# Kernel optimization log

Measured on AMD Instinct MI355X. Metric: run time of the kernel, lower is better.

## Reference

```python
import jax, jax.numpy as jnp
import numpy as np

N = 200_000   # nodes
E = 6_400_000 # edges (avg degree 32)
F = 128       # input features
H = 8         # latent_dim
G = 1024      # graphs in batch


def setup_inputs() -> dict:
    key = jax.random.key(0)
    ks = jax.random.split(key, 8)
    x = jax.random.normal(ks[0], (N, F), dtype=jnp.float32)
    edge_index = jax.random.randint(ks[1], (2, E), 0, N, dtype=jnp.int64)
    batch = jnp.sort(jax.random.randint(ks[2], (N,), 0, G, dtype=jnp.int64))
    W1 = jax.random.normal(ks[3], (F, H), dtype=jnp.float32) * 0.1
    b1 = jnp.zeros((H,), dtype=jnp.float32)
    W2 = jax.random.normal(ks[4], (H, H), dtype=jnp.float32) * 0.1
    b2 = jnp.zeros((H,), dtype=jnp.float32)
    Wl = jax.random.normal(ks[5], (H, 1), dtype=jnp.float32) * 0.1
    bl = jnp.zeros((1,), dtype=jnp.float32)
    return {"x": x, "W1": W1, "b1": b1, "W2": W2, "b2": b2,
            "Wl": Wl, "bl": bl, "edge_index": edge_index,
            "batch": batch, "num_graphs": G}


def gcn_conv(x, W, b, src, dst, n):
    """PyG GCNConv: add self-loops, symmetric deg^{-1/2} normalization,
    scatter-add aggregation, then bias."""
    loop = jnp.arange(n, dtype=src.dtype)
    s = jnp.concatenate([src, loop])
    d = jnp.concatenate([dst, loop])
    deg = jax.ops.segment_sum(jnp.ones_like(d, dtype=x.dtype), d, num_segments=n)
    dinv = jax.lax.rsqrt(deg)  # deg >= 1 thanks to self-loops
    norm = dinv[s] * dinv[d]   # [E+N]
    h = x @ W                  # [N, H] small GEMM
    msg = h[s] * norm[:, None] # irregular gather over edges
    return jax.ops.segment_sum(msg, d, num_segments=n) + b


def reference(x, W1, b1, W2, b2, Wl, bl, edge_index, batch, num_graphs):
    src, dst = edge_index[0], edge_index[1]
    n = x.shape[0]
    h = jax.nn.relu(gcn_conv(x, W1, b1, src, dst, n))
    h = jax.nn.relu(gcn_conv(h, W2, b2, src, dst, n))
    # per-graph node-sum readout (fused segment_sum replaces the torch loop)
    outs = jax.ops.segment_sum(h, batch, num_segments=num_graphs)  # [G, H]
    logits = outs @ Wl + bl  # [G, 1]
    return jax.nn.sigmoid(logits)
```

## Files before the change

kernel.cpp:

```cpp
#include <hip/hip_runtime.h>
#include <hip/hip_bf16.h>
#include <math.h>

#define THREADS 256
#define SHIFT 8
#define B1 512
#define S1T 1024
#define TILE 8192
#define EPT (TILE / S1T)
#define ECAP 10240
#define BCAP ECAP
#define CPT (ECAP / 512)

typedef _Float16 f16x8 __attribute__((ext_vector_type(8)));
typedef float f32x4 __attribute__((ext_vector_type(4)));

#define NTL(p) __builtin_nontemporal_load(p)

static inline size_t A256(size_t x) { return (x + 255) & ~(size_t)255; }

__global__ void init_kernel(int* __restrict__ gcursor, int NBUK) {
    int i = blockIdx.x * blockDim.x + threadIdx.x;
    if (i < NBUK) gcursor[i] = i * ECAP;
}

__global__ __launch_bounds__(S1T) void scatterd_kernel(
        const int* __restrict__ src, const int* __restrict__ dst,
        int* __restrict__ gcursor, int* __restrict__ ebuf, int E, int chunk) {
    __shared__ int cnt[1024];
    __shared__ int texcl[1024];
    __shared__ int runbase[1024];
    __shared__ int wtot[16];
    __shared__ int spk[TILE];
    __shared__ unsigned short sbk[TILE];
    int b = blockIdx.x, t = threadIdx.x;
    int lane = t & 63, wv = t >> 6;
    int lo = b * chunk, hi = min(E, lo + chunk);
    for (int tb = lo; tb < hi; tb += TILE) {
        int tn = min(TILE, hi - tb);
        cnt[t] = 0;
        __syncthreads();
        int pk[EPT], bk[EPT], rk[EPT];
#pragma unroll
        for (int i = 0; i < EPT; ++i) {
            int idx = t + i * S1T;
            if (idx < tn) {
                int e = tb + idx;
                int s = src[e], d = dst[e];
                bk[i] = d >> SHIFT;
                pk[i] = ((d & 255) << 24) | s;
                rk[i] = atomicAdd(&cnt[bk[i]], 1);
            } else bk[i] = -1;
        }
        __syncthreads();
        int v = cnt[t];
        if (v > 0) runbase[t] = atomicAdd(&gcursor[t], v);
        int inc = v;
#pragma unroll
        for (int m = 1; m < 64; m <<= 1) {
            int u = __shfl_up(inc, m, 64);
            if (lane >= m) inc += u;
        }
        if (lane == 63) wtot[wv] = inc;
        __syncthreads();
        int pre = 0;
        for (int j = 0; j < wv; ++j) pre += wtot[j];
        texcl[t] = pre + inc - v;
        __syncthreads();
#pragma unroll
        for (int i = 0; i < EPT; ++i) {
            if (bk[i] >= 0) {
                int p = texcl[bk[i]] + rk[i];
                spk[p] = pk[i];
                sbk[p] = (unsigned short)bk[i];
            }
        }
        __syncthreads();
        for (int j = t; j < tn; j += S1T) {
            int bkt = sbk[j];
            ebuf[runbase[bkt] + (j - texcl[bkt])] = spk[j];
        }
        __syncthreads();
    }
}

__global__ __launch_bounds__(512) void bucket_csr_kernel(
        const int* __restrict__ ebuf, const int* __restrict__ gcursor,
        int* __restrict__ ebuf2, int2* __restrict__ rowinfo,
        float* __restrict__ dinv, int N) {
    __shared__ int cnt[256];
    __shared__ int cur[256];
    __shared__ int wtot[4];
    __shared__ int srt[BCAP];
    int k = blockIdx.x, t = threadIdx.x;
    int lane = t & 63;
    int bs = k * ECAP;
    int n = min(gcursor[k] - bs, BCAP);
    if (t < 256) cnt[t] = 0;
    __syncthreads();
    int p[CPT], rk[CPT];
#pragma unroll
    for (int u = 0; u < CPT; ++u) {
        int i = t + u * 512;
        if (i < n) {
            p[u] = ebuf[bs + i];
            rk[u] = atomicAdd(&cnt[(p[u] >> 24) & 255], 1);
        }
    }
    __syncthreads();
    int myc = 0, inc = 0;
    if (t < 256) {
        myc = cnt[t];
        inc = myc;
#pragma unroll
        for (int m = 1; m < 64; m <<= 1) {
            int u = __shfl_up(inc, m, 64);
            if (lane >= m) inc += u;
        }
        if (lane == 63) wtot[t >> 6] = inc;
    }
    __syncthreads();
    if (t < 256) {
        int pre = 0;
        for (int j = 0; j < (t >> 6); ++j) pre += wtot[j];
        int ex = pre + inc - myc;
        cur[t] = ex;
        int node = (k << SHIFT) + t;
        if (node < N) {
            rowinfo[node] = make_int2(bs + ex, myc);
            dinv[node] = rsqrtf((float)myc + 1.0f);
        }
    }
    __syncthreads();
#pragma unroll
    for (int u = 0; u < CPT; ++u) {
        int i = t + u * 512;
        if (i < n)
            srt[cur[(p[u] >> 24) & 255] + rk[u]] = p[u] & 0xFFFFFF;
    }
    __syncthreads();
    for (int i = t; i < n; i += 512) ebuf2[bs + i] = srt[i];
}

__global__ __launch_bounds__(256) void gemm1_kernel(
        const float* __restrict__ x, const float* __restrict__ W1,
        const float* __restrict__ dinv, f16x8* __restrict__ out, int N) {
    __shared__ float Wt[8 * 128];
    for (int i = threadIdx.x; i < 1024; i += blockDim.x) {
        int f = i >> 3, h = i & 7;
        Wt[h * 128 + f] = W1[i];
    }
    __syncthreads();
    const f32x4* x4 = (const f32x4*)x;
    const f32x4* Wt4 = (const f32x4*)Wt;
    int lane = threadIdx.x & 63;
    int r = lane >> 3;
    int s = lane & 7;
    int wid = (blockIdx.x * blockDim.x + threadIdx.x) >> 6;
    int nw = (gridDim.x * blockDim.x) >> 6;
    int ngroups = (N + 7) >> 3;
    for (int g = wid; g < ngroups; g += nw) {
        int row = g * 8 + r;
        float acc[8] = {0.f, 0.f, 0.f, 0.f, 0.f, 0.f, 0.f, 0.f};
        if (row < N) {
            const f32x4* xp = x4 + (size_t)row * 32 + s;
#pragma unroll
            for (int j = 0; j < 4; ++j) {
                f32x4 v = NTL(xp + j * 8);
#pragma unroll
                for (int h = 0; h < 8; ++h) {
                    f32x4 w = Wt4[h * 32 + j * 8 + s];
                    acc[h] += v[0] * w[0] + v[1] * w[1] + v[2] * w[2] + v[3] * w[3];
                }
            }
        }
#pragma unroll
        for (int m = 4; m >= 1; m >>= 1)
#pragma unroll
            for (int h = 0; h < 8; ++h)
                acc[h] += __shfl_xor(acc[h], m, 64);
        if (s == 0 && row < N) {
            float dd = dinv[row];
            f16x8 o;
#pragma unroll
            for (int h = 0; h < 8; ++h) o[h] = (_Float16)(acc[h] * dd);
            out[row] = o;
        }
    }
}

template <int LAYER>
__global__ __launch_bounds__(512) void gather2_kernel(
        const int* __restrict__ ebuf2, const int* __restrict__ gcursor,
        const int2* __restrict__ rowinfo, const float* __restrict__ dinv,
        const f16x8* __restrict__ hin, const float* __restrict__ bias,
        const float* __restrict__ W2, f16x8* __restrict__ hout, int N) {
    __shared__ int sed[BCAP];
    __shared__ float part[256][9];
    __shared__ float sW[64];
    __shared__ float sb[8];
    int t = threadIdx.x;
    if (LAYER == 1 && t < 64) sW[t] = W2[t];
    if (t < 8) sb[t] = bias[t];
    int k = blockIdx.x;
    int bs = k * ECAP;
    int n = min(gcursor[k] - bs, BCAP);
    for (int i = t; i < n; i += 512) sed[i] = NTL(ebuf2 + bs + i);
    __syncthreads();
    int tn = t & 255;
    int hf = t >> 8;
    int node = (k << SHIFT) + tn;
    float acc[8] = {0.f, 0.f, 0.f, 0.f, 0.f, 0.f, 0.f, 0.f};
    if (node < N) {
        int2 ri = rowinfo[node];
        int nlo = (ri.y + 1) >> 1;
        int base = (hf ? (ri.x + nlo) : ri.x) - bs;
        int cnt = hf ? (ri.y - nlo) : nlo;
        const int* el = sed + base;
        int i = 0;
        for (; i + 8 <= cnt; i += 8) {
            f16x8 a[8];
#pragma unroll
            for (int u = 0; u < 8; ++u) a[u] = hin[el[i + u]];
#pragma unroll
            for (int j = 0; j < 8; ++j) {
                float s0 = (float)a[0][j] + (float)a[1][j];
                float s1 = (float)a[2][j] + (float)a[3][j];
                float s2 = (float)a[4][j] + (float)a[5][j];
                float s3 = (float)a[6][j] + (float)a[7][j];
                acc[j] += (s0 + s1) + (s2 + s3);
            }
        }
        for (; i < cnt; ++i) {
            f16x8 a = hin[el[i]];
#pragma unroll
            for (int j = 0; j < 8; ++j) acc[j] += (float)a[j];
        }
    }
    if (hf) {
#pragma unroll
        for (int j = 0; j < 8; ++j) part[tn][j] = acc[j];
    }
    __syncthreads();
    if (hf || node >= N) return;
#pragma unroll
    for (int j = 0; j < 8; ++j) acc[j] += part[tn][j];
    float dd = dinv[node];
    f16x8 hs = hin[node];
    float v[8];
#pragma unroll
    for (int j = 0; j < 8; ++j)
        v[j] = fmaxf(dd * (acc[j] + (float)hs[j]) + sb[j], 0.f);
    f16x8 o;
    if (LAYER == 1) {
#pragma unroll
        for (int j = 0; j < 8; ++j) {
            float s = 0.f;
#pragma unroll
            for (int kk = 0; kk < 8; ++kk) s += v[kk] * sW[kk * 8 + j];
            o[j] = (_Float16)(s * dd);
        }
    } else {
#pragma unroll
        for (int j = 0; j < 8; ++j) o[j] = (_Float16)v[j];
    }
    hout[node] = o;
}

__global__ void readout_kernel(const f16x8* __restrict__ h2, const int* __restrict__ batch,
                               const float* __restrict__ Wl, const float* __restrict__ bl,
                               float* __restrict__ out, int N) {
    __shared__ int sbnd[2];
    __shared__ float part[4][8];
    int g = blockIdx.x;
    int t = threadIdx.x;
    if (t < 2) {
        int target = g + t;
        int lo = 0, hi = N;
        while (lo < hi) {
            int mid = (lo + hi) >> 1;
            if (batch[mid] < target) lo = mid + 1; else hi = mid;
        }
        sbnd[t] = lo;
    }
    __syncthreads();
    int lo = sbnd[0], hi = sbnd[1];
    float s[8] = {0.f, 0.f, 0.f, 0.f, 0.f, 0.f, 0.f, 0.f};
    for (int i = lo + t; i < hi; i += 256) {
        f16x8 a = h2[i];
#pragma unroll
        for (int o = 0; o < 8; ++o) s[o] += (float)a[o];
    }
#pragma unroll
    for (int m = 32; m >= 1; m >>= 1)
#pragma unroll
        for (int o = 0; o < 8; ++o) s[o] += __shfl_xor(s[o], m, 64);
    int wv = t >> 6;
    if ((t & 63) == 0)
#pragma unroll
        for (int o = 0; o < 8; ++o) part[wv][o] = s[o];
    __syncthreads();
    if (t == 0) {
        float accv = bl[0];
#pragma unroll
        for (int o = 0; o < 8; ++o)
            accv += (part[0][o] + part[1][o] + part[2][o] + part[3][o]) * Wl[o];
        out[g] = 1.f / (1.f + expf(-accv));
    }
}

extern "C" void kernel_launch(void* const* d_in, const int* in_sizes, int n_in,
                              void* d_out, int out_size, void* d_ws, size_t ws_size,
                              hipStream_t stream) {
    const float* x  = (const float*)d_in[0];
    const float* W1 = (const float*)d_in[1];
    const float* b1 = (const float*)d_in[2];
    const float* W2 = (const float*)d_in[3];
    const float* b2 = (const float*)d_in[4];
    const float* Wl = (const float*)d_in[5];
    const float* bl = (const float*)d_in[6];
    const int* ei    = (const int*)d_in[7];
    const int* batch = (const int*)d_in[8];

    const int N = in_sizes[8];
    const int E = in_sizes[7] / 2;
    const int G = out_size;
    const int* src = ei;
    const int* dst = ei + E;

    const int NBUK = (N + 255) >> SHIFT;
    const int chunk = (E + B1 - 1) / B1;

    char* ws = (char*)d_ws;
    size_t off = 0;
    size_t o_gcur   = off; off = A256(off + (size_t)NBUK * 4);
    size_t o_dinv   = off; off = A256(off + (size_t)N * 4);
    size_t o_rowinf = off; off = A256(off + (size_t)N * 8);
    size_t o_hbufA  = off; off = A256(off + (size_t)N * 16);
    size_t o_hbufB  = off; off = A256(off + (size_t)N * 16);
    size_t o_ebuf   = off; off = A256(off + (size_t)NBUK * ECAP * 4);
    size_t o_ebuf2  = off; off = A256(off + (size_t)NBUK * ECAP * 4);

    int*   gcursor = (int*)(ws + o_gcur);
    float* dinv    = (float*)(ws + o_dinv);
    int2*  rowinf  = (int2*)(ws + o_rowinf);
    f16x8* hbufA   = (f16x8*)(ws + o_hbufA);
    f16x8* hbufB   = (f16x8*)(ws + o_hbufB);
    int*   ebuf    = (int*)(ws + o_ebuf);
    int*   ebuf2   = (int*)(ws + o_ebuf2);

    init_kernel<<<1, 1024, 0, stream>>>(gcursor, NBUK);
    scatterd_kernel<<<B1, S1T, 0, stream>>>(src, dst, gcursor, ebuf, E, chunk);

    bucket_csr_kernel<<<NBUK, 512, 0, stream>>>(ebuf, gcursor, ebuf2, rowinf, dinv, N);

    gemm1_kernel<<<4096, THREADS, 0, stream>>>(x, W1, dinv, hbufA, N);

    gather2_kernel<1><<<NBUK, 512, 0, stream>>>(ebuf2, gcursor, rowinf, dinv, hbufA, b1, W2, hbufB, N);
    gather2_kernel<2><<<NBUK, 512, 0, stream>>>(ebuf2, gcursor, rowinf, dinv, hbufB, b2, W2, hbufA, N);

    readout_kernel<<<G, 256, 0, stream>>>(hbufA, batch, Wl, bl, (float*)d_out, N);
}
```

Baseline: 185.3 us.

## Enlarge scatter tile, add nontemporal edge-buffer traffic, vectorize edge staging

Raises the scatter kernel's per-iteration tile from 8192 to 13312 edges, moving its staging arrays into dynamic shared memory, so each block needs fewer tile passes and global-cursor atomics. Writes and reads of the intermediate edge buffers switch to nontemporal stores and loads. The gather kernel stages its edge list into LDS with 16-byte vector loads plus a scalar tail. The larger tile raises LDS use (about 78 KB dynamic plus static) and register pressure from the EPT2=13 per-thread arrays, which may cut occupancy. The vector loads also depend on bs being 16-byte aligned.

```diff
diff --git a/kernel.cpp b/kernel.cpp
--- a/kernel.cpp
+++ b/kernel.cpp
@@ -6,16 +6,18 @@
 #define SHIFT 8
 #define B1 512
 #define S1T 1024
-#define TILE 8192
-#define EPT (TILE / S1T)
+#define TILE2 13312
+#define EPT2 (TILE2 / S1T)
 #define ECAP 10240
 #define BCAP ECAP
 #define CPT (ECAP / 512)
 
 typedef _Float16 f16x8 __attribute__((ext_vector_type(8)));
 typedef float f32x4 __attribute__((ext_vector_type(4)));
+typedef int i32x4 __attribute__((ext_vector_type(4)));
 
 #define NTL(p) __builtin_nontemporal_load(p)
+#define NTS(p, v) __builtin_nontemporal_store((v), (p))
 
 static inline size_t A256(size_t x) { return (x + 255) & ~(size_t)255; }
 
@@ -31,18 +33,19 @@
     __shared__ int texcl[1024];
     __shared__ int runbase[1024];
     __shared__ int wtot[16];
-    __shared__ int spk[TILE];
-    __shared__ unsigned short sbk[TILE];
+    extern __shared__ int dynls[];
+    int* spk = dynls;
+    unsigned short* sbk = (unsigned short*)(spk + TILE2);
     int b = blockIdx.x, t = threadIdx.x;
     int lane = t & 63, wv = t >> 6;
     int lo = b * chunk, hi = min(E, lo + chunk);
-    for (int tb = lo; tb < hi; tb += TILE) {
-        int tn = min(TILE, hi - tb);
+    for (int tb = lo; tb < hi; tb += TILE2) {
+        int tn = min(TILE2, hi - tb);
         cnt[t] = 0;
         __syncthreads();
-        int pk[EPT], bk[EPT], rk[EPT];
-#pragma unroll
-        for (int i = 0; i < EPT; ++i) {
+        int pk[EPT2], bk[EPT2], rk[EPT2];
+#pragma unroll
+        for (int i = 0; i < EPT2; ++i) {
             int idx = t + i * S1T;
             if (idx < tn) {
                 int e = tb + idx;
@@ -68,7 +71,7 @@
         texcl[t] = pre + inc - v;
         __syncthreads();
 #pragma unroll
-        for (int i = 0; i < EPT; ++i) {
+        for (int i = 0; i < EPT2; ++i) {
             if (bk[i] >= 0) {
                 int p = texcl[bk[i]] + rk[i];
                 spk[p] = pk[i];
@@ -78,7 +81,7 @@
         __syncthreads();
         for (int j = t; j < tn; j += S1T) {
             int bkt = sbk[j];
-            ebuf[runbase[bkt] + (j - texcl[bkt])] = spk[j];
+            NTS(&ebuf[runbase[bkt] + (j - texcl[bkt])], spk[j]);
         }
         __syncthreads();
     }
@@ -103,7 +106,7 @@
     for (int u = 0; u < CPT; ++u) {
         int i = t + u * 512;
         if (i < n) {
-            p[u] = ebuf[bs + i];
+            p[u] = NTL(ebuf + bs + i);
             rk[u] = atomicAdd(&cnt[(p[u] >> 24) & 255], 1);
         }
     }
@@ -139,7 +142,7 @@
             srt[cur[(p[u] >> 24) & 255] + rk[u]] = p[u] & 0xFFFFFF;
     }
     __syncthreads();
-    for (int i = t; i < n; i += 512) ebuf2[bs + i] = srt[i];
+    for (int i = t; i < n; i += 512) NTS(&ebuf2[bs + i], srt[i]);
 }
 
 __global__ __launch_bounds__(256) void gemm1_kernel(
@@ -205,7 +208,13 @@
     int k = blockIdx.x;
     int bs = k * ECAP;
     int n = min(gcursor[k] - bs, BCAP);
-    for (int i = t; i < n; i += 512) sed[i] = NTL(ebuf2 + bs + i);
+    {
+        int n4 = n >> 2;
+        const i32x4* e4 = (const i32x4*)(ebuf2 + bs);
+        i32x4* s4 = (i32x4*)sed;
+        for (int i = t; i < n4; i += 512) s4[i] = NTL(e4 + i);
+        for (int i = (n4 << 2) + t; i < n; i += 512) sed[i] = NTL(ebuf2 + bs + i);
+    }
     __syncthreads();
     int tn = t & 255;
     int hf = t >> 8;
@@ -349,8 +358,10 @@
     int*   ebuf    = (int*)(ws + o_ebuf);
     int*   ebuf2   = (int*)(ws + o_ebuf2);
 
+    const size_t dynbytes = (size_t)TILE2 * 4 + (size_t)TILE2 * 2;
+
     init_kernel<<<1, 1024, 0, stream>>>(gcursor, NBUK);
-    scatterd_kernel<<<B1, S1T, 0, stream>>>(src, dst, gcursor, ebuf, E, chunk);
+    scatterd_kernel<<<B1, S1T, dynbytes, stream>>>(src, dst, gcursor, ebuf, E, chunk);
 
     bucket_csr_kernel<<<NBUK, 512, 0, stream>>>(ebuf, gcursor, ebuf2, rowinf, dinv, N);
 
```

Measured after the change: 189.6 us. 2.3% more time.
